# Kernel optimization log

Hardware: AMD Instinct MI355X
Metric: run time of the kernel (lower is better)

The kernel has to match this reference:

```python
import jax, jax.numpy as jnp
import numpy as np

N = 50000  # num nodes


def _spmm(edge_index, edge_w, x):
    # sparse [N,N] @ dense [N,d] via gather + segment-sum
    row, col = edge_index[0], edge_index[1]
    msgs = edge_w[:, None] * x[col]                      # [E, d]
    return jax.ops.segment_sum(msgs, row, num_segments=N)


def setup_inputs() -> dict:
    key = jax.random.key(0)
    k1, k2, k3, k4, k5 = jax.random.split(key, 5)
    E1, E2, d = 800000, 1600000, 128
    x = jax.random.normal(k1, (N, d), dtype=jnp.float32)
    edge_index1 = jax.random.randint(k2, (2, E1), 0, N, dtype=jnp.int64)
    edge_w1 = jax.random.uniform(k3, (E1,), dtype=jnp.float32)
    edge_index2 = jax.random.randint(k4, (2, E2), 0, N, dtype=jnp.int64)
    edge_w2 = jax.random.uniform(k5, (E2,), dtype=jnp.float32)
    return {"x": x, "edge_index1": edge_index1, "edge_w1": edge_w1,
            "edge_index2": edge_index2, "edge_w2": edge_w2}


def reference(x, edge_index1, edge_w1, edge_index2, edge_w2):
    x1 = _spmm(edge_index1, edge_w1, x)   # adj_t  @ x  -> [N, d]
    x2 = _spmm(edge_index2, edge_w2, x)   # adj_t2 @ x  -> [N, d]
    return jnp.concatenate([x1, x2], axis=1)  # [N, 2d]
```

## Files before the change

### kernel.cpp

```cpp
#include <hip/hip_runtime.h>


#define N_NODES 50000
#define D 128
#define OUT_STRIDE 256

#define BSHIFT 6
#define BROWS (1 << BSHIFT)
#define NBUCK ((N_NODES + BROWS - 1) >> BSHIFT)
#define CHUNK 9216
#define CAPB 3072

typedef float vf2 __attribute__((ext_vector_type(2)));

static inline size_t align256(size_t x) { return (x + 255) & ~(size_t)255; }

__device__ __forceinline__ unsigned f32_to_bf16_bits(float f) {
    unsigned u = __float_as_uint(f);
    return (u + 0x7fffu + ((u >> 16) & 1u)) >> 16;
}


__global__ void __launch_bounds__(512) bin_scatter(
        const int* __restrict__ ei1, const float* __restrict__ w1, int E1, int nch1,
        const int* __restrict__ ei2, const float* __restrict__ w2, int E2,
        uint2* __restrict__ inter, int* __restrict__ ends) {
    int cid = blockIdx.x;
    int g = (cid < nch1) ? 0 : 1;
    int chunk = g ? cid - nch1 : cid;
    const int*   ei = g ? ei2 : ei1;
    const float* w  = g ? w2  : w1;
    int E           = g ? E2  : E1;
    int e0  = chunk * CHUNK;
    int cnt = min(CHUNK, E - e0);

    __shared__ uint2 stage[CHUNK];
    __shared__ int cntb[NBUCK], cur[NBUCK];
    __shared__ int wsum[8];
    int t = threadIdx.x, lane = t & 63, wid = t >> 6;
    for (int b = t; b < NBUCK; b += 512) cntb[b] = 0;
    __syncthreads();
    for (int i = t; i < cnt; i += 512)
        atomicAdd(&cntb[ei[e0 + i] >> BSHIFT], 1);
    __syncthreads();
    {
        int i0 = 2 * t;
        int v0 = (i0     < NBUCK) ? cntb[i0]     : 0;
        int v1 = (i0 + 1 < NBUCK) ? cntb[i0 + 1] : 0;
        int p = v0 + v1, s = p;
        #pragma unroll
        for (int d = 1; d < 64; d <<= 1) { int u = __shfl_up(s, d, 64); if (lane >= d) s += u; }
        if (lane == 63) wsum[wid] = s;
        __syncthreads();
        int add = 0;
        #pragma unroll
        for (int k = 0; k < 8; ++k) if (k < wid) add += wsum[k];
        s += add;
        int e = s - p;
        if (i0     < NBUCK) cur[i0]     = e;
        if (i0 + 1 < NBUCK) cur[i0 + 1] = e + v0;
    }
    __syncthreads();
    for (int i = t; i < cnt; i += 512) {
        int row = ei[e0 + i];
        int col = ei[E + e0 + i];
        unsigned rec = (unsigned)col | (f32_to_bf16_bits(w[e0 + i]) << 16);
        int b = row >> BSHIFT;
        int pos = atomicAdd(&cur[b], 1);
        stage[pos] = make_uint2((unsigned)(row & (BROWS - 1)), rec);
    }
    __syncthreads();
    for (int b = t; b < NBUCK; b += 512)
        ends[(size_t)cid * NBUCK + b] = cur[b];
    for (int i = t; i < cnt; i += 512)
        inter[(size_t)cid * CHUNK + i] = stage[i];
}


__global__ void cvt_bf16(const float* __restrict__ x, uint2* __restrict__ xb4, int n4) {
    int i = blockIdx.x * blockDim.x + threadIdx.x;
    if (i >= n4) return;
    float4 v = ((const float4*)x)[i];
    unsigned a = f32_to_bf16_bits(v.x);
    unsigned b = f32_to_bf16_bits(v.y);
    unsigned c = f32_to_bf16_bits(v.z);
    unsigned d = f32_to_bf16_bits(v.w);
    xb4[i] = make_uint2(a | (b << 16), c | (d << 16));
}


__device__ __forceinline__ void fma_rec(unsigned p, unsigned rec, float& ax, float& ay) {
    float w = __int_as_float((int)(rec & 0xffff0000u));
    ax += w * __int_as_float((int)(p << 16));
    ay += w * __int_as_float((int)(p & 0xffff0000u));
}

__global__ void __launch_bounds__(512, 4) bucket_accum(
        const uint2* __restrict__ inter, const int* __restrict__ ends,
        const unsigned* __restrict__ xb,
        float* __restrict__ out, int nch1, int nch2) {
    int b = blockIdx.x, g = blockIdx.y;
    int c0 = g ? nch1 : 0;
    int nc = g ? nch2 : nch1;

    __shared__ unsigned char rl[CAPB];
    __shared__ unsigned recs[CAPB];
    __shared__ unsigned outb[CAPB];
    __shared__ int crow[BROWS], cur[BROWS], rstart[BROWS];
    __shared__ int total;
    int t = threadIdx.x, lane = t & 63, wid = t >> 6;
    if (t < BROWS) crow[t] = 0;
    if (t == 0) total = 0;
    __syncthreads();
    for (int ci = t; ci < nc; ci += 512) {
        const int* ep = ends + (size_t)(c0 + ci) * NBUCK;
        int s = b ? ep[b - 1] : 0;
        int e = ep[b];
        int n = e - s;
        if (!n) continue;
        int dst = atomicAdd(&total, n);
        const uint2* src = inter + (size_t)(c0 + ci) * CHUNK + s;
        int k = 0;
        for (; k + 2 <= n; k += 2) {
            uint2 a  = src[k];
            uint2 b2 = src[k + 1];
            int p0 = dst + k, p1 = dst + k + 1;
            if (p0 < CAPB) { rl[p0] = (unsigned char)a.x;  recs[p0] = a.y;  atomicAdd(&crow[a.x], 1); }
            if (p1 < CAPB) { rl[p1] = (unsigned char)b2.x; recs[p1] = b2.y; atomicAdd(&crow[b2.x], 1); }
        }
        if (k < n) {
            uint2 a = src[k];
            int p0 = dst + k;
            if (p0 < CAPB) { rl[p0] = (unsigned char)a.x; recs[p0] = a.y; atomicAdd(&crow[a.x], 1); }
        }
    }
    __syncthreads();
    int cnt = min(total, CAPB);
    if (wid == 0) {
        int v = crow[lane], s = v;
        #pragma unroll
        for (int d = 1; d < 64; d <<= 1) { int u = __shfl_up(s, d, 64); if (lane >= d) s += u; }
        cur[lane] = s - v;
        rstart[lane] = s - v;
    }
    __syncthreads();
    for (int i = t; i < cnt; i += 512) {
        int pos = atomicAdd(&cur[rl[i]], 1);
        outb[pos] = recs[i];
    }
    __syncthreads();
    for (int r = wid * 8; r < wid * 8 + 8; ++r) {
        int grow = (b << BSHIFT) + r;
        if (grow >= N_NODES) break;
        int s0 = rstart[r], e0 = cur[r];
        float ax = 0.f, ay = 0.f;
        int j = s0;
        for (; j + 4 <= e0; j += 4) {
            unsigned c0r = outb[j];
            unsigned c1 = outb[j + 1];
            unsigned c2 = outb[j + 2];
            unsigned c3 = outb[j + 3];
            unsigned p0 = xb[(size_t)(c0r & 0xffffu) * 64 + lane];
            unsigned p1 = xb[(size_t)(c1 & 0xffffu) * 64 + lane];
            unsigned p2 = xb[(size_t)(c2 & 0xffffu) * 64 + lane];
            unsigned p3 = xb[(size_t)(c3 & 0xffffu) * 64 + lane];
            fma_rec(p0, c0r, ax, ay);
            fma_rec(p1, c1, ax, ay);
            fma_rec(p2, c2, ax, ay);
            fma_rec(p3, c3, ax, ay);
        }
        for (; j < e0; ++j) {
            unsigned c = outb[j];
            unsigned p = xb[(size_t)(c & 0xffffu) * 64 + lane];
            fma_rec(p, c, ax, ay);
        }
        vf2 rv; rv.x = ax; rv.y = ay;
        vf2* o = (vf2*)(out + (size_t)grow * OUT_STRIDE + g * D);
        __builtin_nontemporal_store(rv, o + lane);
    }
}


__global__ void spmm_scatter(const float* __restrict__ x,
                             const int* __restrict__ ei,
                             const float* __restrict__ w,
                             float* __restrict__ out,
                             int E, int col_off) {
    long long gid = (long long)blockIdx.x * blockDim.x + threadIdx.x;
    int e    = (int)(gid >> 5);
    int lane = (int)(gid & 31);
    if (e >= E) return;
    int row  = ei[e];
    int col  = ei[E + e];
    float wv = w[e];
    const float4* xv = (const float4*)(x + (size_t)col * D);
    float4 v = xv[lane];
    float* o = out + (size_t)row * OUT_STRIDE + col_off + lane * 4;
    atomicAdd(o + 0, wv * v.x);
    atomicAdd(o + 1, wv * v.y);
    atomicAdd(o + 2, wv * v.z);
    atomicAdd(o + 3, wv * v.w);
}

extern "C" void kernel_launch(void* const* d_in, const int* in_sizes, int n_in,
                              void* d_out, int out_size, void* d_ws, size_t ws_size,
                              hipStream_t stream) {
    const float* x   = (const float*)d_in[0];
    const int*   ei1 = (const int*)d_in[1];
    const float* w1  = (const float*)d_in[2];
    const int*   ei2 = (const int*)d_in[3];
    const float* w2  = (const float*)d_in[4];
    float* out = (float*)d_out;

    const int E1 = in_sizes[1] / 2;
    const int E2 = in_sizes[3] / 2;
    const int block = 256;

    int nch1 = (E1 + CHUNK - 1) / CHUNK;
    int nch2 = (E2 + CHUNK - 1) / CHUNK;
    int ncht = nch1 + nch2;

    size_t ends_b  = align256((size_t)ncht * NBUCK * sizeof(int));
    size_t inter_b = align256((size_t)ncht * CHUNK * sizeof(uint2));
    size_t xb_b    = align256((size_t)N_NODES * 64 * sizeof(unsigned));
    size_t o_ends  = 0;
    size_t o_int   = o_ends + ends_b;
    size_t o_xb    = o_int + inter_b;
    size_t needed  = o_xb + xb_b;

    if (ws_size < needed) {
        (void)hipMemsetAsync(d_out, 0, (size_t)out_size * sizeof(float), stream);
        long long th1 = (long long)E1 * 32;
        spmm_scatter<<<(int)((th1 + block - 1) / block), block, 0, stream>>>(
            x, ei1, w1, out, E1, 0);
        long long th2 = (long long)E2 * 32;
        spmm_scatter<<<(int)((th2 + block - 1) / block), block, 0, stream>>>(
            x, ei2, w2, out, E2, D);
        return;
    }

    char* ws = (char*)d_ws;
    int*      ends  = (int*)(ws + o_ends);
    uint2*    inter = (uint2*)(ws + o_int);
    unsigned* xb    = (unsigned*)(ws + o_xb);

    {
        int n4 = N_NODES * 32;
        cvt_bf16<<<(n4 + block - 1) / block, block, 0, stream>>>(
            x, (uint2*)xb, n4);
    }

    bin_scatter<<<ncht, 512, 0, stream>>>(
        ei1, w1, E1, nch1, ei2, w2, E2, inter, ends);

    {
        dim3 g(NBUCK, 2);
        bucket_accum<<<g, 512, 0, stream>>>(inter, ends, xb, out, nch1, nch2);
    }
}
```

Before: 212.1 us.

## Replace shared-memory atomics with wave-match ballots in binning and bucket accumulation

Both binning kernels switch from LDS atomic counters to ballot-based wave matching: each wave computes per-bucket ranks among lanes, keeps per-wave histograms, and writes records without atomics. The ends array is transposed to bucket-major so bucket_accum can load segment bounds coalesced. bucket_accum now puts records into fixed per-wave per-row cells with a small spill buffer, then gathers them into a per-row scratch list, avoiding the atomic count/prefix/scatter passes. The trade-off is many ballots per element (10 or 6 bits), plus fixed caps (CELLCAP, RSCR, SPILLCAP) that silently drop edges if rows have high degree.

```diff
diff --git a/kernel.cpp b/kernel.cpp
--- a/kernel.cpp
+++ b/kernel.cpp
@@ -6,10 +6,14 @@
 #define OUT_STRIDE 256
 
 #define BSHIFT 6
-#define BROWS (1 << BSHIFT)
+#define BROWS 64
 #define NBUCK ((N_NODES + BROWS - 1) >> BSHIFT)
+#define BBITS 10
 #define CHUNK 9216
-#define CAPB 3072
+#define WSEG (CHUNK / 8)
+#define CELLCAP 16
+#define RSCR 96
+#define SPILLCAP 128
 
 typedef float vf2 __attribute__((ext_vector_type(2)));
 
@@ -20,11 +24,22 @@
     return (u + 0x7fffu + ((u >> 16) & 1u)) >> 16;
 }
 
+template<int BITS>
+__device__ __forceinline__ unsigned long long wave_match(int v, bool valid) {
+    unsigned long long m = __ballot(valid ? 1 : 0);
+    #pragma unroll
+    for (int k = 0; k < BITS; ++k) {
+        unsigned long long vb = __ballot((v >> k) & 1);
+        m &= ((v >> k) & 1) ? vb : ~vb;
+    }
+    return m;
+}
+
 
 __global__ void __launch_bounds__(512) bin_scatter(
         const int* __restrict__ ei1, const float* __restrict__ w1, int E1, int nch1,
         const int* __restrict__ ei2, const float* __restrict__ w2, int E2,
-        uint2* __restrict__ inter, int* __restrict__ ends) {
+        uint2* __restrict__ inter, int* __restrict__ ends, int ncht) {
     int cid = blockIdx.x;
     int g = (cid < nch1) ? 0 : 1;
     int chunk = g ? cid - nch1 : cid;
@@ -35,43 +50,77 @@
     int cnt = min(CHUNK, E - e0);
 
     __shared__ uint2 stage[CHUNK];
-    __shared__ int cntb[NBUCK], cur[NBUCK];
+    __shared__ int hwc[8][NBUCK];
     __shared__ int wsum[8];
     int t = threadIdx.x, lane = t & 63, wid = t >> 6;
-    for (int b = t; b < NBUCK; b += 512) cntb[b] = 0;
-    __syncthreads();
-    for (int i = t; i < cnt; i += 512)
-        atomicAdd(&cntb[ei[e0 + i] >> BSHIFT], 1);
+    unsigned long long below = (1ull << lane) - 1ull;
+    for (int i = t; i < 8 * NBUCK; i += 512) ((int*)hwc)[i] = 0;
+    __syncthreads();
+
+    int s0 = wid * WSEG, s1 = min(cnt, s0 + WSEG);
+    for (int i0 = s0; i0 < s1; i0 += 64) {
+        int i = i0 + lane;
+        bool v = (i < s1);
+        int row = v ? ei[e0 + i] : 0;
+        int bb = row >> BSHIFT;
+        unsigned long long m = wave_match<BBITS>(bb, v);
+        if (v && (m & below) == 0)
+            hwc[wid][bb] += __popcll(m);
+    }
     __syncthreads();
     {
-        int i0 = 2 * t;
-        int v0 = (i0     < NBUCK) ? cntb[i0]     : 0;
-        int v1 = (i0 + 1 < NBUCK) ? cntb[i0 + 1] : 0;
-        int p = v0 + v1, s = p;
+        int b0 = 2 * t, b1 = 2 * t + 1;
+        int h0[8], h1[8];
+        int t0 = 0, t1 = 0;
+        if (b0 < NBUCK) {
+            #pragma unroll
+            for (int q = 0; q < 8; ++q) { h0[q] = hwc[q][b0]; t0 += h0[q]; }
+        }
+        if (b1 < NBUCK) {
+            #pragma unroll
+            for (int q = 0; q < 8; ++q) { h1[q] = hwc[q][b1]; t1 += h1[q]; }
+        }
+        int p = t0 + t1, s = p;
         #pragma unroll
-        for (int d = 1; d < 64; d <<= 1) { int u = __shfl_up(s, d, 64); if (lane >= d) s += u; }
+        for (int d2 = 1; d2 < 64; d2 <<= 1) { int u = __shfl_up(s, d2, 64); if (lane >= d2) s += u; }
         if (lane == 63) wsum[wid] = s;
         __syncthreads();
         int add = 0;
         #pragma unroll
         for (int k = 0; k < 8; ++k) if (k < wid) add += wsum[k];
         s += add;
-        int e = s - p;
-        if (i0     < NBUCK) cur[i0]     = e;
-        if (i0 + 1 < NBUCK) cur[i0 + 1] = e + v0;
-    }
-    __syncthreads();
-    for (int i = t; i < cnt; i += 512) {
-        int row = ei[e0 + i];
-        int col = ei[E + e0 + i];
-        unsigned rec = (unsigned)col | (f32_to_bf16_bits(w[e0 + i]) << 16);
-        int b = row >> BSHIFT;
-        int pos = atomicAdd(&cur[b], 1);
-        stage[pos] = make_uint2((unsigned)(row & (BROWS - 1)), rec);
-    }
-    __syncthreads();
-    for (int b = t; b < NBUCK; b += 512)
-        ends[(size_t)cid * NBUCK + b] = cur[b];
+        int excl = s - p;
+        if (b0 < NBUCK) {
+            int a = excl;
+            #pragma unroll
+            for (int q = 0; q < 8; ++q) { hwc[q][b0] = a; a += h0[q]; }
+            ends[(size_t)b0 * ncht + cid] = a;
+        }
+        if (b1 < NBUCK) {
+            int a = excl + t0;
+            #pragma unroll
+            for (int q = 0; q < 8; ++q) { hwc[q][b1] = a; a += h1[q]; }
+            ends[(size_t)b1 * ncht + cid] = a;
+        }
+    }
+    __syncthreads();
+    for (int i0 = s0; i0 < s1; i0 += 64) {
+        int i = i0 + lane;
+        bool v = (i < s1);
+        int row = v ? ei[e0 + i] : 0;
+        int col = v ? ei[E + e0 + i] : 0;
+        float wv = v ? w[e0 + i] : 0.f;
+        int bb = row >> BSHIFT;
+        unsigned long long m = wave_match<BBITS>(bb, v);
+        if (v) {
+            int rank = __popcll(m & below);
+            int base = hwc[wid][bb];
+            stage[base + rank] = make_uint2((unsigned)(row & (BROWS - 1)),
+                                            (unsigned)col | (f32_to_bf16_bits(wv) << 16));
+            if (rank == 0) hwc[wid][bb] = base + __popcll(m);
+        }
+    }
+    __syncthreads();
     for (int i = t; i < cnt; i += 512)
         inter[(size_t)cid * CHUNK + i] = stage[i];
 }
@@ -98,81 +147,105 @@
 __global__ void __launch_bounds__(512, 4) bucket_accum(
         const uint2* __restrict__ inter, const int* __restrict__ ends,
         const unsigned* __restrict__ xb,
-        float* __restrict__ out, int nch1, int nch2) {
+        float* __restrict__ out, int nch1, int nch2, int ncht) {
     int b = blockIdx.x, g = blockIdx.y;
     int c0 = g ? nch1 : 0;
     int nc = g ? nch2 : nch1;
 
-    __shared__ unsigned char rl[CAPB];
-    __shared__ unsigned recs[CAPB];
-    __shared__ unsigned outb[CAPB];
-    __shared__ int crow[BROWS], cur[BROWS], rstart[BROWS];
-    __shared__ int total;
+    __shared__ unsigned region[8][BROWS][CELLCAP];
+    __shared__ int cwi[8][BROWS];
+    __shared__ uint2 spill[SPILLCAP];
+    __shared__ int sp_cnt;
+    __shared__ unsigned scratch[8][RSCR];
+
     int t = threadIdx.x, lane = t & 63, wid = t >> 6;
-    if (t < BROWS) crow[t] = 0;
-    if (t == 0) total = 0;
-    __syncthreads();
-    for (int ci = t; ci < nc; ci += 512) {
-        const int* ep = ends + (size_t)(c0 + ci) * NBUCK;
-        int s = b ? ep[b - 1] : 0;
-        int e = ep[b];
-        int n = e - s;
-        if (!n) continue;
-        int dst = atomicAdd(&total, n);
-        const uint2* src = inter + (size_t)(c0 + ci) * CHUNK + s;
-        int k = 0;
-        for (; k + 2 <= n; k += 2) {
-            uint2 a  = src[k];
-            uint2 b2 = src[k + 1];
-            int p0 = dst + k, p1 = dst + k + 1;
-            if (p0 < CAPB) { rl[p0] = (unsigned char)a.x;  recs[p0] = a.y;  atomicAdd(&crow[a.x], 1); }
-            if (p1 < CAPB) { rl[p1] = (unsigned char)b2.x; recs[p1] = b2.y; atomicAdd(&crow[b2.x], 1); }
-        }
-        if (k < n) {
-            uint2 a = src[k];
-            int p0 = dst + k;
-            if (p0 < CAPB) { rl[p0] = (unsigned char)a.x; recs[p0] = a.y; atomicAdd(&crow[a.x], 1); }
-        }
-    }
-    __syncthreads();
-    int cnt = min(total, CAPB);
-    if (wid == 0) {
-        int v = crow[lane], s = v;
+    unsigned long long below = (1ull << lane) - 1ull;
+    for (int i = t; i < 8 * BROWS; i += 512) ((int*)cwi)[i] = 0;
+    if (t == 0) sp_cnt = 0;
+    __syncthreads();
+
+    const int* eb  = ends + (size_t)b * ncht + c0;
+    const int* ebp = eb - ncht;
+    int er0, er1, er2, sr0, sr1, sr2;
+    { int ci = lane;       bool v = ci < nc; er0 = v ? eb[ci] : 0; sr0 = (v && b) ? ebp[ci] : 0; }
+    { int ci = lane + 64;  bool v = ci < nc; er1 = v ? eb[ci] : 0; sr1 = (v && b) ? ebp[ci] : 0; }
+    { int ci = lane + 128; bool v = ci < nc; er2 = v ? eb[ci] : 0; sr2 = (v && b) ? ebp[ci] : 0; }
+
+    for (int ci = wid; ci < nc; ci += 8) {
+        int slot = ci >> 6, sl = ci & 63;
+        int ev = (slot == 0) ? er0 : (slot == 1) ? er1 : er2;
+        int svv = (slot == 0) ? sr0 : (slot == 1) ? sr1 : sr2;
+        int segs = __shfl(svv, sl, 64);
+        int sege = __shfl(ev, sl, 64);
+        int segn = sege - segs;
+        const uint2* src = inter + (size_t)(c0 + ci) * CHUNK + segs;
+        for (int k0 = 0; k0 < segn; k0 += 64) {
+            int k = k0 + lane;
+            bool v = (k < segn);
+            uint2 r = v ? src[k] : make_uint2(0u, 0u);
+            int row = (int)(r.x & 63u);
+            unsigned long long m = wave_match<6>(row, v);
+            if (v) {
+                int rank = __popcll(m & below);
+                int base = cwi[wid][row];
+                int pos = base + rank;
+                if (pos < CELLCAP) {
+                    region[wid][row][pos] = r.y;
+                } else {
+                    int sp = atomicAdd(&sp_cnt, 1);
+                    if (sp < SPILLCAP) spill[sp] = make_uint2((unsigned)row, r.y);
+                }
+                if (rank == 0) cwi[wid][row] = base + __popcll(m);
+            }
+        }
+    }
+    __syncthreads();
+    int spn = min(sp_cnt, SPILLCAP);
+
+    for (int r8 = 0; r8 < 8; ++r8) {
+        int row = wid * 8 + r8;
+        int grow = (b << BSHIFT) + row;
+        if (grow >= N_NODES) break;
+        int cw[8];
+        int tot = 0;
         #pragma unroll
-        for (int d = 1; d < 64; d <<= 1) { int u = __shfl_up(s, d, 64); if (lane >= d) s += u; }
-        cur[lane] = s - v;
-        rstart[lane] = s - v;
-    }
-    __syncthreads();
-    for (int i = t; i < cnt; i += 512) {
-        int pos = atomicAdd(&cur[rl[i]], 1);
-        outb[pos] = recs[i];
-    }
-    __syncthreads();
-    for (int r = wid * 8; r < wid * 8 + 8; ++r) {
-        int grow = (b << BSHIFT) + r;
-        if (grow >= N_NODES) break;
-        int s0 = rstart[r], e0 = cur[r];
+        for (int q = 0; q < 8; ++q) { cw[q] = min(cwi[q][row], CELLCAP); tot += cw[q]; }
+        int tt = min(tot, RSCR);
+        if (lane < tt) {
+            int off = lane, w8 = 0;
+            #pragma unroll
+            for (int q = 0; q < 7; ++q)
+                if (w8 == q && off >= cw[q]) { off -= cw[q]; w8 = q + 1; }
+            scratch[wid][lane] = region[w8][row][off];
+        }
+        int tt2 = tt;
+        for (int s2 = 0; s2 < spn; ++s2) {
+            uint2 sv2 = spill[s2];
+            if ((int)sv2.x == row && tt2 < RSCR) {
+                if (lane == 0) scratch[wid][tt2] = sv2.y;
+                ++tt2;
+            }
+        }
         float ax = 0.f, ay = 0.f;
-        int j = s0;
-        for (; j + 4 <= e0; j += 4) {
-            unsigned c0r = outb[j];
-            unsigned c1 = outb[j + 1];
-            unsigned c2 = outb[j + 2];
-            unsigned c3 = outb[j + 3];
+        int j = 0;
+        for (; j + 4 <= tt2; j += 4) {
+            unsigned c0r = scratch[wid][j];
+            unsigned c1r = scratch[wid][j + 1];
+            unsigned c2r = scratch[wid][j + 2];
+            unsigned c3r = scratch[wid][j + 3];
             unsigned p0 = xb[(size_t)(c0r & 0xffffu) * 64 + lane];
-            unsigned p1 = xb[(size_t)(c1 & 0xffffu) * 64 + lane];
-            unsigned p2 = xb[(size_t)(c2 & 0xffffu) * 64 + lane];
-            unsigned p3 = xb[(size_t)(c3 & 0xffffu) * 64 + lane];
+            unsigned p1 = xb[(size_t)(c1r & 0xffffu) * 64 + lane];
+            unsigned p2 = xb[(size_t)(c2r & 0xffffu) * 64 + lane];
+            unsigned p3 = xb[(size_t)(c3r & 0xffffu) * 64 + lane];
             fma_rec(p0, c0r, ax, ay);
-            fma_rec(p1, c1, ax, ay);
-            fma_rec(p2, c2, ax, ay);
-            fma_rec(p3, c3, ax, ay);
-        }
-        for (; j < e0; ++j) {
-            unsigned c = outb[j];
-            unsigned p = xb[(size_t)(c & 0xffffu) * 64 + lane];
-            fma_rec(p, c, ax, ay);
+            fma_rec(p1, c1r, ax, ay);
+            fma_rec(p2, c2r, ax, ay);
+            fma_rec(p3, c3r, ax, ay);
+        }
+        for (; j < tt2; ++j) {
+            unsigned cr = scratch[wid][j];
+            unsigned p = xb[(size_t)(cr & 0xffffu) * 64 + lane];
+            fma_rec(p, cr, ax, ay);
         }
         vf2 rv; rv.x = ax; rv.y = ay;
         vf2* o = (vf2*)(out + (size_t)grow * OUT_STRIDE + g * D);
@@ -220,7 +293,7 @@
     int nch2 = (E2 + CHUNK - 1) / CHUNK;
     int ncht = nch1 + nch2;
 
-    size_t ends_b  = align256((size_t)ncht * NBUCK * sizeof(int));
+    size_t ends_b  = align256((size_t)NBUCK * ncht * sizeof(int));
     size_t inter_b = align256((size_t)ncht * CHUNK * sizeof(uint2));
     size_t xb_b    = align256((size_t)N_NODES * 64 * sizeof(unsigned));
     size_t o_ends  = 0;
@@ -251,10 +324,10 @@
     }
 
     bin_scatter<<<ncht, 512, 0, stream>>>(
-        ei1, w1, E1, nch1, ei2, w2, E2, inter, ends);
+        ei1, w1, E1, nch1, ei2, w2, E2, inter, ends, ncht);
 
     {
-        dim3 g(NBUCK, 2);
-        bucket_accum<<<g, 512, 0, stream>>>(inter, ends, xb, out, nch1, nch2);
-    }
-}
+        dim3 gr(NBUCK, 2);
+        bucket_accum<<<gr, 512, 0, stream>>>(inter, ends, xb, out, nch1, nch2, ncht);
+    }
+}
```

Result: slower. 256.5 us (+20.9%).

## Fuse bf16 conversion into binning kernel and replace LDS atomics with wave-match ranking

Applied to the files above, without the earlier changes.

Merges the separate bf16 conversion kernel into the binning kernel as extra blocks, which removes one launch and lets the two run concurrently. The binning pass now reads each edge once into registers. Per-wave bucket histograms are built with ballot-based matching instead of shared-memory atomics, and the staging positions come from a per-wave prefix. CHUNK drops to 8192 so the work splits evenly across waves. A guard on the chunk count is added, and the extra ballot loop costs more ALU per edge.

```diff
diff --git a/kernel.cpp b/kernel.cpp
--- a/kernel.cpp
+++ b/kernel.cpp
@@ -6,9 +6,12 @@
 #define OUT_STRIDE 256
 
 #define BSHIFT 6
-#define BROWS (1 << BSHIFT)
+#define BROWS 64
 #define NBUCK ((N_NODES + BROWS - 1) >> BSHIFT)
-#define CHUNK 9216
+#define BBITS 10
+#define CHUNK 8192
+#define WSEG (CHUNK / 8)
+#define SITERS (WSEG / 64)
 #define CAPB 3072
 
 typedef float vf2 __attribute__((ext_vector_type(2)));
@@ -20,12 +23,37 @@
     return (u + 0x7fffu + ((u >> 16) & 1u)) >> 16;
 }
 
-
-__global__ void __launch_bounds__(512) bin_scatter(
+template<int BITS>
+__device__ __forceinline__ unsigned long long wave_match(int v, bool valid) {
+    unsigned long long m = __ballot(valid ? 1 : 0);
+    #pragma unroll
+    for (int k = 0; k < BITS; ++k) {
+        unsigned long long vb = __ballot((v >> k) & 1);
+        m &= ((v >> k) & 1) ? vb : ~vb;
+    }
+    return m;
+}
+
+
+__global__ void __launch_bounds__(512, 4) prep(
         const int* __restrict__ ei1, const float* __restrict__ w1, int E1, int nch1,
-        const int* __restrict__ ei2, const float* __restrict__ w2, int E2,
-        uint2* __restrict__ inter, int* __restrict__ ends) {
-    int cid = blockIdx.x;
+        const int* __restrict__ ei2, const float* __restrict__ w2, int E2, int ncht,
+        uint2* __restrict__ inter, int* __restrict__ ends,
+        const float* __restrict__ x, uint2* __restrict__ xb4, int n4) {
+    int bid = blockIdx.x;
+    if (bid >= ncht) {
+        int i = (bid - ncht) * 512 + threadIdx.x;
+        if (i < n4) {
+            float4 v = ((const float4*)x)[i];
+            unsigned a = f32_to_bf16_bits(v.x);
+            unsigned b = f32_to_bf16_bits(v.y);
+            unsigned c = f32_to_bf16_bits(v.z);
+            unsigned d = f32_to_bf16_bits(v.w);
+            xb4[i] = make_uint2(a | (b << 16), c | (d << 16));
+        }
+        return;
+    }
+    int cid = bid;
     int g = (cid < nch1) ? 0 : 1;
     int chunk = g ? cid - nch1 : cid;
     const int*   ei = g ? ei2 : ei1;
@@ -35,57 +63,84 @@
     int cnt = min(CHUNK, E - e0);
 
     __shared__ uint2 stage[CHUNK];
-    __shared__ int cntb[NBUCK], cur[NBUCK];
+    __shared__ unsigned short hwc[8][NBUCK];
     __shared__ int wsum[8];
     int t = threadIdx.x, lane = t & 63, wid = t >> 6;
-    for (int b = t; b < NBUCK; b += 512) cntb[b] = 0;
-    __syncthreads();
-    for (int i = t; i < cnt; i += 512)
-        atomicAdd(&cntb[ei[e0 + i] >> BSHIFT], 1);
+    unsigned long long below = (1ull << lane) - 1ull;
+    for (int i = t; i < (8 * NBUCK) / 2; i += 512) ((int*)hwc)[i] = 0;
+    __syncthreads();
+
+    int s0 = wid * WSEG, s1 = min(cnt, s0 + WSEG);
+    unsigned meta[SITERS];
+    unsigned recs[SITERS];
+    #pragma unroll
+    for (int k = 0; k < SITERS; ++k) {
+        int i = s0 + k * 64 + lane;
+        bool v = (i < s1);
+        int row = v ? ei[e0 + i] : 0;
+        int col = v ? ei[E + e0 + i] : 0;
+        float wv = v ? w[e0 + i] : 0.f;
+        int bb = row >> BSHIFT;
+        unsigned long long m = wave_match<BBITS>(bb, v);
+        unsigned rank = (unsigned)__popcll(m & below);
+        unsigned base = hwc[wid][bb];
+        if (v && (m & below) == 0)
+            hwc[wid][bb] = (unsigned short)(base + (unsigned)__popcll(m));
+        meta[k] = (unsigned)bb | ((unsigned)(row & 63) << 10) | ((base + rank) << 16);
+        recs[k] = (unsigned)col | (f32_to_bf16_bits(wv) << 16);
+    }
     __syncthreads();
     {
-        int i0 = 2 * t;
-        int v0 = (i0     < NBUCK) ? cntb[i0]     : 0;
-        int v1 = (i0 + 1 < NBUCK) ? cntb[i0 + 1] : 0;
-        int p = v0 + v1, s = p;
+        int b0 = 2 * t, b1 = b0 + 1;
+        int h0[8], h1[8];
+        int t0 = 0, t1 = 0;
+        if (b0 < NBUCK) {
+            #pragma unroll
+            for (int q = 0; q < 8; ++q) { h0[q] = hwc[q][b0]; t0 += h0[q]; }
+        }
+        if (b1 < NBUCK) {
+            #pragma unroll
+            for (int q = 0; q < 8; ++q) { h1[q] = hwc[q][b1]; t1 += h1[q]; }
+        }
+        int p = t0 + t1, s = p;
         #pragma unroll
-        for (int d = 1; d < 64; d <<= 1) { int u = __shfl_up(s, d, 64); if (lane >= d) s += u; }
+        for (int d2 = 1; d2 < 64; d2 <<= 1) { int u = __shfl_up(s, d2, 64); if (lane >= d2) s += u; }
         if (lane == 63) wsum[wid] = s;
         __syncthreads();
         int add = 0;
         #pragma unroll
         for (int k = 0; k < 8; ++k) if (k < wid) add += wsum[k];
         s += add;
-        int e = s - p;
-        if (i0     < NBUCK) cur[i0]     = e;
-        if (i0 + 1 < NBUCK) cur[i0 + 1] = e + v0;
-    }
-    __syncthreads();
-    for (int i = t; i < cnt; i += 512) {
-        int row = ei[e0 + i];
-        int col = ei[E + e0 + i];
-        unsigned rec = (unsigned)col | (f32_to_bf16_bits(w[e0 + i]) << 16);
-        int b = row >> BSHIFT;
-        int pos = atomicAdd(&cur[b], 1);
-        stage[pos] = make_uint2((unsigned)(row & (BROWS - 1)), rec);
-    }
-    __syncthreads();
-    for (int b = t; b < NBUCK; b += 512)
-        ends[(size_t)cid * NBUCK + b] = cur[b];
+        int excl = s - p;
+        if (b0 < NBUCK) {
+            int a = excl;
+            #pragma unroll
+            for (int q = 0; q < 8; ++q) { int h = h0[q]; hwc[q][b0] = (unsigned short)a; a += h; }
+            ends[(size_t)cid * NBUCK + b0] = a;
+        }
+        if (b1 < NBUCK) {
+            int a = excl + t0;
+            #pragma unroll
+            for (int q = 0; q < 8; ++q) { int h = h1[q]; hwc[q][b1] = (unsigned short)a; a += h; }
+            ends[(size_t)cid * NBUCK + b1] = a;
+        }
+    }
+    __syncthreads();
+    #pragma unroll
+    for (int k = 0; k < SITERS; ++k) {
+        int i = s0 + k * 64 + lane;
+        if (i < s1) {
+            unsigned mk = meta[k];
+            unsigned bb = mk & 1023u;
+            unsigned rlv = (mk >> 10) & 63u;
+            unsigned pos = mk >> 16;
+            unsigned base = hwc[wid][bb];
+            stage[base + pos] = make_uint2(rlv, recs[k]);
+        }
+    }
+    __syncthreads();
     for (int i = t; i < cnt; i += 512)
         inter[(size_t)cid * CHUNK + i] = stage[i];
-}
-
-
-__global__ void cvt_bf16(const float* __restrict__ x, uint2* __restrict__ xb4, int n4) {
-    int i = blockIdx.x * blockDim.x + threadIdx.x;
-    if (i >= n4) return;
-    float4 v = ((const float4*)x)[i];
-    unsigned a = f32_to_bf16_bits(v.x);
-    unsigned b = f32_to_bf16_bits(v.y);
-    unsigned c = f32_to_bf16_bits(v.z);
-    unsigned d = f32_to_bf16_bits(v.w);
-    xb4[i] = make_uint2(a | (b << 16), c | (d << 16));
 }
 
 
@@ -228,7 +283,9 @@
     size_t o_xb    = o_int + inter_b;
     size_t needed  = o_xb + xb_b;
 
-    if (ws_size < needed) {
+    bool ok = (nch1 <= 512) && (nch2 <= 512);
+
+    if (ws_size < needed || !ok) {
         (void)hipMemsetAsync(d_out, 0, (size_t)out_size * sizeof(float), stream);
         long long th1 = (long long)E1 * 32;
         spmm_scatter<<<(int)((th1 + block - 1) / block), block, 0, stream>>>(
@@ -246,15 +303,14 @@
 
     {
         int n4 = N_NODES * 32;
-        cvt_bf16<<<(n4 + block - 1) / block, block, 0, stream>>>(
-            x, (uint2*)xb, n4);
-    }
-
-    bin_scatter<<<ncht, 512, 0, stream>>>(
-        ei1, w1, E1, nch1, ei2, w2, E2, inter, ends);
+        int ncvt = (n4 + 511) / 512;
+        prep<<<ncht + ncvt, 512, 0, stream>>>(
+            ei1, w1, E1, nch1, ei2, w2, E2, ncht,
+            inter, ends, x, (uint2*)xb, n4);
+    }
 
     {
-        dim3 g(NBUCK, 2);
-        bucket_accum<<<g, 512, 0, stream>>>(inter, ends, xb, out, nch1, nch2);
-    }
-}
+        dim3 gr(NBUCK, 2);
+        bucket_accum<<<gr, 512, 0, stream>>>(inter, ends, xb, out, nch1, nch2);
+    }
+}
```

Result: no change. 212.9 us (+0.4%).
